# Optimization experiments

Hardware: AMD Instinct MI355X
Metric: run time of the kernel (lower is better)

Reference implementation:

```python
import jax, jax.numpy as jnp
import numpy as np

EMBED = 512
HEADS = 8
HEAD_DIM = EMBED // HEADS
N, T = 512, 64


def setup_inputs() -> dict:
    key = jax.random.key(0)
    ks = jax.random.split(key, 11)
    s = 1.0 / np.sqrt(EMBED)
    inp = {
        'values': jax.random.normal(ks[0], (N, T, EMBED), jnp.float32),
        'keys':   jax.random.normal(ks[1], (N, T, EMBED), jnp.float32),
        'query':  jax.random.normal(ks[2], (N, T, EMBED), jnp.float32),
        'Wv': jax.random.uniform(ks[3], (EMBED, EMBED), jnp.float32, -s, s),
        'bv': jax.random.uniform(ks[4], (EMBED,), jnp.float32, -s, s),
        'Wk': jax.random.uniform(ks[5], (EMBED, EMBED), jnp.float32, -s, s),
        'bk': jax.random.uniform(ks[6], (EMBED,), jnp.float32, -s, s),
        'Wq': jax.random.uniform(ks[7], (EMBED, EMBED), jnp.float32, -s, s),
        'bq': jax.random.uniform(ks[8], (EMBED,), jnp.float32, -s, s),
        'Wo': jax.random.uniform(ks[9], (EMBED, EMBED), jnp.float32, -s, s),
        'bo': jax.random.uniform(ks[10], (EMBED,), jnp.float32, -s, s),
    }
    return inp


def reference(values, keys, query, Wv, bv, Wk, bk, Wq, bq, Wo, bo):
    n, t, c = query.shape
    v = (values @ Wv.T + bv).reshape(n, t, HEADS, HEAD_DIM)
    k = (keys   @ Wk.T + bk).reshape(n, t, HEADS, HEAD_DIM)
    q = (query  @ Wq.T + bq).reshape(n, t, HEADS, HEAD_DIM)
    # attention over the batch axis: energy[q,k,t,h]
    energy = jnp.einsum('qthd,kthd->qkth', q, k)
    attn = jax.nn.softmax(energy / jnp.sqrt(jnp.float32(EMBED)), axis=1)
    out = jnp.einsum('qkth,kthd->qthd', attn, v).reshape(n, t, HEADS * HEAD_DIM)
    return out @ Wo.T + bo
```

## Files before the change

### kernel.cpp

```cpp
#include <hip/hip_runtime.h>
#include <hip/hip_bf16.h>
#include <math.h>

#define NBATCH 512
#define TT 64
#define EMB 512
#define NHEADS 8
#define HDIM 64
#define MROWS (NBATCH * TT)
#define ROWSTRIDE (TT * EMB)
#define WSEG 262144

static constexpr float QSCALE = 0.0637587140f;

typedef __attribute__((ext_vector_type(8))) short short8v;
typedef __attribute__((ext_vector_type(4))) float f32x4;

__device__ __forceinline__ unsigned short f2bf(float x) {
    union { float f; unsigned int u; } v; v.f = x;
    unsigned int r = v.u + 0x7fff + ((v.u >> 16) & 1);
    return (unsigned short)(r >> 16);
}

__device__ __forceinline__ unsigned int cvtpk(float lo, float hi) {
    unsigned int r;
    asm("v_cvt_pk_bf16_f32 %0, %1, %2" : "=v"(r) : "v"(lo), "v"(hi));
    return r;
}

__device__ __forceinline__ void gl16(const void* g, void* l) {
    __builtin_amdgcn_global_load_lds(
        (const __attribute__((address_space(1))) unsigned int*)g,
        (__attribute__((address_space(3))) unsigned int*)l, 16, 0, 0);
}

__global__ __launch_bounds__(256) void cvtw(
    const float* __restrict__ w0, const float* __restrict__ w1,
    const float* __restrict__ w2, const float* __restrict__ w3,
    unsigned short* __restrict__ dst)
{
    const int seg = blockIdx.y;
    const float* src = (seg == 0) ? w0 : (seg == 1) ? w1 : (seg == 2) ? w2 : w3;
    const float sc = (seg == 0) ? QSCALE : 1.0f;
    const size_t i = (size_t)blockIdx.x * 256 + threadIdx.x;
    float4 v = reinterpret_cast<const float4*>(src)[i];
    ushort4 r;
    r.x = f2bf(v.x * sc); r.y = f2bf(v.y * sc); r.z = f2bf(v.z * sc); r.w = f2bf(v.w * sc);
    reinterpret_cast<ushort4*>(dst + (size_t)seg * WSEG)[i] = r;
}

__global__ __launch_bounds__(512) void gemm_proj3(
    const float* __restrict__ A0, const float* __restrict__ A1,
    const float* __restrict__ A2, const unsigned short* __restrict__ Wb,
    const float* __restrict__ b0, const float* __restrict__ b1, const float* __restrict__ b2,
    unsigned short* __restrict__ o0, unsigned short* __restrict__ o1, unsigned short* __restrict__ o2)
{
    __shared__ __align__(16) float Asf[128 * 64];
    __shared__ __align__(16) unsigned short Bs[512 * 64];
    const int z = blockIdx.y;
    const float* A = (z == 0) ? A0 : (z == 1) ? A1 : A2;
    const unsigned short* W = Wb + (size_t)z * WSEG;
    const float* bias = (z == 0) ? b0 : (z == 1) ? b1 : b2;
    const float bsc = (z == 0) ? QSCALE : 1.0f;
    unsigned short* Cout = (z == 0) ? o0 : (z == 1) ? o1 : o2;

    const int tid = threadIdx.x;
    const int wave = tid >> 6, lane = tid & 63;
    const int lg = lane >> 4, li = lane & 15;
    const int m0 = blockIdx.x * 128;
    const int wm = (wave >> 2) * 64;
    const int wn = (wave & 3) * 128;

    f32x4 acc[4][8] = {};

    const int au = (tid & 15) ^ ((tid >> 4) & 15);
    const float* gaf = A + (size_t)(m0 + (tid >> 4)) * 512 + au * 4;
    float* lA = Asf + wave * 256;
    const unsigned short* gb = W + (size_t)(tid >> 3) * 512 + (tid & 7) * 8;
    unsigned short* lB = Bs + wave * 512;

    for (int k0 = 0; k0 < 512; k0 += 64) {
        __syncthreads();
#pragma unroll
        for (int i = 0; i < 4; i++)
            gl16(gaf + k0 + (size_t)i * 32 * 512, lA + i * 2048);
#pragma unroll
        for (int i = 0; i < 8; i++)
            gl16(gb + k0 + (size_t)i * 64 * 512, lB + i * 4096);
        __syncthreads();

#pragma unroll
        for (int kk = 0; kk < 2; kk++) {
            short8v af[4];
#pragma unroll
            for (int i = 0; i < 4; i++) {
                const int r = wm + i * 16 + li;
                const int lu0 = kk * 8 + lg * 2;
                const float4 fa = *reinterpret_cast<const float4*>(
                    &Asf[r * 64 + (lu0 ^ li) * 4]);
                const float4 fb = *reinterpret_cast<const float4*>(
                    &Asf[r * 64 + ((lu0 + 1) ^ li) * 4]);
                union { unsigned int u[4]; short8v v; } pk;
                pk.u[0] = cvtpk(fa.x, fa.y); pk.u[1] = cvtpk(fa.z, fa.w);
                pk.u[2] = cvtpk(fb.x, fb.y); pk.u[3] = cvtpk(fb.z, fb.w);
                af[i] = pk.v;
            }
#pragma unroll
            for (int j = 0; j < 8; j++) {
                const short8v bfr = *reinterpret_cast<const short8v*>(
                    &Bs[(wn + j * 16 + li) * 64 + kk * 32 + lg * 8]);
#pragma unroll
                for (int i = 0; i < 4; i++)
                    acc[i][j] = __builtin_amdgcn_mfma_f32_16x16x32_bf16(af[i], bfr, acc[i][j], 0, 0, 0);
            }
        }
    }

#pragma unroll
    for (int j = 0; j < 8; j++) {
        const int col = wn + j * 16 + li;
        const float bb = bias[col] * bsc;
#pragma unroll
        for (int i = 0; i < 4; i++) {
            const int row0 = m0 + wm + i * 16 + lg * 4;
#pragma unroll
            for (int r = 0; r < 4; r++)
                Cout[(size_t)(row0 + r) * 512 + col] = f2bf(acc[i][j][r] + bb);
        }
    }
}

__global__ __launch_bounds__(256) void gemm_out(
    const unsigned short* __restrict__ A, const unsigned short* __restrict__ W,
    const float* __restrict__ bias, float* __restrict__ Cout)
{
    __shared__ __align__(16) unsigned short As[128 * 32];
    __shared__ __align__(16) unsigned short Bs[128 * 32];
    const int tid = threadIdx.x;
    const int wave = tid >> 6, lane = tid & 63;
    const int lg = lane >> 4, li = lane & 15;
    const int m0 = blockIdx.x * 128;
    const int n0 = blockIdx.y * 128;
    const int wr = (wave >> 1) * 64;
    const int wc = (wave & 1) * 64;

    f32x4 acc[4][4] = {};

    const unsigned short* ga = A + (size_t)(m0 + (tid >> 2)) * 512 + (tid & 3) * 8;
    const unsigned short* gb = W + (size_t)(n0 + (tid >> 2)) * 512 + (tid & 3) * 8;
    unsigned short* lA = &As[wave * 512];
    unsigned short* lB = &Bs[wave * 512];

    for (int k0 = 0; k0 < 512; k0 += 32) {
        __syncthreads();
        gl16(ga + k0, lA);
        gl16(ga + k0 + 64 * 512, lA + 2048);
        gl16(gb + k0, lB);
        gl16(gb + k0 + 64 * 512, lB + 2048);
        __syncthreads();

        short8v af[4], bfr[4];
#pragma unroll
        for (int i = 0; i < 4; i++) {
            af[i]  = *reinterpret_cast<const short8v*>(&As[(wr + i * 16 + li) * 32 + lg * 8]);
            bfr[i] = *reinterpret_cast<const short8v*>(&Bs[(wc + i * 16 + li) * 32 + lg * 8]);
        }
#pragma unroll
        for (int i = 0; i < 4; i++)
#pragma unroll
            for (int j = 0; j < 4; j++)
                acc[i][j] = __builtin_amdgcn_mfma_f32_16x16x32_bf16(af[i], bfr[j], acc[i][j], 0, 0, 0);
    }

#pragma unroll
    for (int j = 0; j < 4; j++) {
        const int col = n0 + wc + j * 16 + li;
        const float bb = bias[col];
#pragma unroll
        for (int i = 0; i < 4; i++) {
            const int row0 = m0 + wr + i * 16 + lg * 4;
#pragma unroll
            for (int r = 0; r < 4; r++)
                Cout[(size_t)(row0 + r) * 512 + col] = acc[i][j][r] + bb;
        }
    }
}

__global__ __launch_bounds__(256) void attn_bf16(
    const unsigned short* __restrict__ qp, const unsigned short* __restrict__ kp,
    const unsigned short* __restrict__ vp, unsigned short* __restrict__ ao)
{
    __shared__ __align__(16) unsigned short Qs[128 * 64];
    __shared__ __align__(16) unsigned short Ks[64 * 64];
    __shared__ __align__(16) unsigned short Vt[64][68];
    __shared__ __align__(16) unsigned short Pl[4][32][72];

    const int tid = threadIdx.x;
    const int wave = tid >> 6, lane = tid & 63;
    const int lg = lane >> 4, li = lane & 15;
    const int n0 = blockIdx.x * 128;
    const int th = blockIdx.y;
    const size_t base = (size_t)(th >> 3) * EMB + (size_t)(th & 7) * HDIM;

    {
        const unsigned short* gq = qp + (size_t)(n0 + (tid >> 3)) * ROWSTRIDE + base + (tid & 7) * 8;
        unsigned short* lq = &Qs[wave * 512];
#pragma unroll
        for (int i = 0; i < 4; i++)
            gl16(gq + (size_t)i * 32 * ROWSTRIDE, lq + i * 2048);
    }
    __syncthreads();
    short8v qf[2][2];
#pragma unroll
    for (int mf = 0; mf < 2; mf++)
#pragma unroll
        for (int kf = 0; kf < 2; kf++)
            qf[mf][kf] = *reinterpret_cast<const short8v*>(
                &Qs[(wave * 32 + mf * 16 + li) * 64 + kf * 32 + lg * 8]);

    const int vd0 = (tid & 15) * 4;
    const int vk0 = (tid >> 4) * 4;
    const unsigned short* gv = vp + base + vd0;
    uint2 vl[4];
#pragma unroll
    for (int i = 0; i < 4; i++)
        vl[i] = *reinterpret_cast<const uint2*>(gv + (size_t)(vk0 + i) * ROWSTRIDE);

    const short8v ones = (short8v)(short)0x3F80;
    f32x4 acc[2][4] = {};
    f32x4 acc_l[2] = {};

    for (int kv = 0; kv < 8; kv++) {
        const int k0 = kv * 64;
        __syncthreads();

        {
            unsigned short* lk = &Ks[wave * 512];
#pragma unroll
            for (int i = 0; i < 2; i++) {
                const int r = (tid >> 3) + i * 32;
                const int srcofs = (((tid & 7) * 8) ^ ((r & 7) * 8));
                gl16(kp + (size_t)(k0 + r) * ROWSTRIDE + base + srcofs, lk + i * 2048);
            }
        }
#pragma unroll
        for (int dd = 0; dd < 4; dd++) {
            const unsigned int sel = (dd & 1) ? 0x07060302u : 0x05040100u;
            const unsigned int a = (dd < 2) ? vl[0].x : vl[0].y;
            const unsigned int b = (dd < 2) ? vl[1].x : vl[1].y;
            const unsigned int c = (dd < 2) ? vl[2].x : vl[2].y;
            const unsigned int d = (dd < 2) ? vl[3].x : vl[3].y;
            uint2 o;
            o.x = __builtin_amdgcn_perm(b, a, sel);
            o.y = __builtin_amdgcn_perm(d, c, sel);
            *reinterpret_cast<uint2*>(&Vt[vd0 + dd][vk0]) = o;
        }
        __syncthreads();

        if (kv < 7) {
#pragma unroll
            for (int i = 0; i < 4; i++)
                vl[i] = *reinterpret_cast<const uint2*>(
                    gv + (size_t)(k0 + 64 + vk0 + i) * ROWSTRIDE);
        }

        f32x4 s[2][4] = {};
#pragma unroll
        for (int nf = 0; nf < 4; nf++) {
            const int key = nf * 16 + li;
#pragma unroll
            for (int kf = 0; kf < 2; kf++) {
                const short8v kfrag = *reinterpret_cast<const short8v*>(
                    &Ks[key * 64 + ((kf * 32 + lg * 8) ^ ((key & 7) * 8))]);
#pragma unroll
                for (int mf = 0; mf < 2; mf++)
                    s[mf][nf] = __builtin_amdgcn_mfma_f32_16x16x32_bf16(kfrag, qf[mf][kf], s[mf][nf], 0, 0, 0);
            }
        }

#pragma unroll
        for (int mf = 0; mf < 2; mf++)
#pragma unroll
            for (int nf = 0; nf < 4; nf++) {
                const float p0 = exp2f(s[mf][nf][0]);
                const float p1 = exp2f(s[mf][nf][1]);
                const float p2 = exp2f(s[mf][nf][2]);
                const float p3 = exp2f(s[mf][nf][3]);
                union { unsigned int u[2]; uint2 v; } pk2;
                pk2.u[0] = cvtpk(p0, p1);
                pk2.u[1] = cvtpk(p2, p3);
                *reinterpret_cast<uint2*>(&Pl[wave][mf * 16 + li][nf * 16 + lg * 4]) = pk2.v;
            }

        short8v pf[2][2];
#pragma unroll
        for (int mf = 0; mf < 2; mf++)
#pragma unroll
            for (int kf = 0; kf < 2; kf++)
                pf[mf][kf] = *reinterpret_cast<const short8v*>(
                    &Pl[wave][mf * 16 + li][kf * 32 + lg * 8]);
#pragma unroll
        for (int mf = 0; mf < 2; mf++)
#pragma unroll
            for (int kf = 0; kf < 2; kf++)
                acc_l[mf] = __builtin_amdgcn_mfma_f32_16x16x32_bf16(pf[mf][kf], ones, acc_l[mf], 0, 0, 0);

#pragma unroll
        for (int df = 0; df < 4; df++)
#pragma unroll
            for (int kf = 0; kf < 2; kf++) {
                const short8v vfr = *reinterpret_cast<const short8v*>(
                    &Vt[df * 16 + li][kf * 32 + lg * 8]);
#pragma unroll
                for (int mf = 0; mf < 2; mf++)
                    acc[mf][df] = __builtin_amdgcn_mfma_f32_16x16x32_bf16(pf[mf][kf], vfr, acc[mf][df], 0, 0, 0);
            }
    }

#pragma unroll
    for (int mf = 0; mf < 2; mf++) {
#pragma unroll
        for (int r = 0; r < 4; r++) {
            const float linv = 1.0f / acc_l[mf][r];
            const int qrow = n0 + wave * 32 + mf * 16 + lg * 4 + r;
#pragma unroll
            for (int df = 0; df < 4; df++)
                ao[(size_t)qrow * ROWSTRIDE + base + df * 16 + li] = f2bf(acc[mf][df][r] * linv);
        }
    }
}

extern "C" void kernel_launch(void* const* d_in, const int* in_sizes, int n_in,
                              void* d_out, int out_size, void* d_ws, size_t ws_size,
                              hipStream_t stream) {
    const float* values = (const float*)d_in[0];
    const float* keys   = (const float*)d_in[1];
    const float* query  = (const float*)d_in[2];
    const float* Wv = (const float*)d_in[3];
    const float* bv = (const float*)d_in[4];
    const float* Wk = (const float*)d_in[5];
    const float* bk = (const float*)d_in[6];
    const float* Wq = (const float*)d_in[7];
    const float* bq = (const float*)d_in[8];
    const float* Wo = (const float*)d_in[9];
    const float* bo = (const float*)d_in[10];
    float* out = (float*)d_out;

    unsigned short* ws16 = (unsigned short*)d_ws;
    const size_t PLANE = (size_t)MROWS * EMB;
    unsigned short* qb = ws16;
    unsigned short* kb = ws16 + PLANE;
    unsigned short* vb = ws16 + 2 * PLANE;
    unsigned short* ab = ws16 + 3 * PLANE;
    unsigned short* wb = ws16 + 4 * PLANE;

    cvtw<<<dim3(WSEG / 4 / 256, 4), 256, 0, stream>>>(Wq, Wk, Wv, Wo, wb);

    gemm_proj3<<<dim3(MROWS / 128, 3), 512, 0, stream>>>(
        query, keys, values, wb, bq, bk, bv, qb, kb, vb);

    attn_bf16<<<dim3(4, TT * NHEADS), 256, 0, stream>>>(qb, kb, vb, ab);

    gemm_out<<<dim3(MROWS / 128, EMB / 128), 256, 0, stream>>>(
        ab, wb + 3 * WSEG, bo, out);
}
```

Before: 223.8 us.

## Double-buffer projection GEMM with register-prefetched bf16 A tiles

Restructures the fused QKV projection GEMM main loop to use K=32 double-buffered LDS tiles. The next W tile is prefetched asynchronously and the next A tile goes through registers while MFMAs run on the current buffer. A is now converted to bf16 once when stored to LDS rather than converted from fp32 on every fragment read, which halves A's LDS footprint. Each iteration now needs one barrier instead of two, so global loads overlap with compute, at the cost of more register pressure and more, smaller loop iterations.

Result: slower. 228.7 us (+2.2%).

```diff
diff --git a/kernel.cpp b/kernel.cpp
--- a/kernel.cpp
+++ b/kernel.cpp
@@ -55,8 +55,8 @@
     const float* __restrict__ b0, const float* __restrict__ b1, const float* __restrict__ b2,
     unsigned short* __restrict__ o0, unsigned short* __restrict__ o1, unsigned short* __restrict__ o2)
 {
-    __shared__ __align__(16) float Asf[128 * 64];
-    __shared__ __align__(16) unsigned short Bs[512 * 64];
+    __shared__ __align__(16) unsigned short Ws[2][512 * 32];
+    __shared__ __align__(16) unsigned short Ab[2][128 * 32];
     const int z = blockIdx.y;
     const float* A = (z == 0) ? A0 : (z == 1) ? A1 : A2;
     const unsigned short* W = Wb + (size_t)z * WSEG;
@@ -73,47 +73,63 @@
 
     f32x4 acc[4][8] = {};
 
-    const int au = (tid & 15) ^ ((tid >> 4) & 15);
-    const float* gaf = A + (size_t)(m0 + (tid >> 4)) * 512 + au * 4;
-    float* lA = Asf + wave * 256;
-    const unsigned short* gb = W + (size_t)(tid >> 3) * 512 + (tid & 7) * 8;
-    unsigned short* lB = Bs + wave * 512;
-
-    for (int k0 = 0; k0 < 512; k0 += 64) {
-        __syncthreads();
+    const unsigned short* gw = W + (size_t)(tid >> 2) * 512
+                             + (size_t)(((tid & 3) ^ ((tid >> 2) & 3))) * 8;
+    const float* ga = A + (size_t)(m0 + (tid >> 2)) * 512 + (tid & 3) * 8;
+    const int awr = tid >> 2;
+    const int awu = (tid & 3) ^ (awr & 3);
+
+    {
 #pragma unroll
         for (int i = 0; i < 4; i++)
-            gl16(gaf + k0 + (size_t)i * 32 * 512, lA + i * 2048);
-#pragma unroll
-        for (int i = 0; i < 8; i++)
-            gl16(gb + k0 + (size_t)i * 64 * 512, lB + i * 4096);
-        __syncthreads();
-
-#pragma unroll
-        for (int kk = 0; kk < 2; kk++) {
-            short8v af[4];
-#pragma unroll
-            for (int i = 0; i < 4; i++) {
-                const int r = wm + i * 16 + li;
-                const int lu0 = kk * 8 + lg * 2;
-                const float4 fa = *reinterpret_cast<const float4*>(
-                    &Asf[r * 64 + (lu0 ^ li) * 4]);
-                const float4 fb = *reinterpret_cast<const float4*>(
-                    &Asf[r * 64 + ((lu0 + 1) ^ li) * 4]);
-                union { unsigned int u[4]; short8v v; } pk;
-                pk.u[0] = cvtpk(fa.x, fa.y); pk.u[1] = cvtpk(fa.z, fa.w);
-                pk.u[2] = cvtpk(fb.x, fb.y); pk.u[3] = cvtpk(fb.z, fb.w);
-                af[i] = pk.v;
-            }
-#pragma unroll
-            for (int j = 0; j < 8; j++) {
-                const short8v bfr = *reinterpret_cast<const short8v*>(
-                    &Bs[(wn + j * 16 + li) * 64 + kk * 32 + lg * 8]);
-#pragma unroll
-                for (int i = 0; i < 4; i++)
-                    acc[i][j] = __builtin_amdgcn_mfma_f32_16x16x32_bf16(af[i], bfr, acc[i][j], 0, 0, 0);
-            }
-        }
+            gl16(gw + (size_t)i * 128 * 512, &Ws[0][wave * 512 + i * 4096]);
+        const float4 f0 = *reinterpret_cast<const float4*>(ga);
+        const float4 f1 = *reinterpret_cast<const float4*>(ga + 4);
+        union { unsigned int u[4]; short8v v; } pk;
+        pk.u[0] = cvtpk(f0.x, f0.y); pk.u[1] = cvtpk(f0.z, f0.w);
+        pk.u[2] = cvtpk(f1.x, f1.y); pk.u[3] = cvtpk(f1.z, f1.w);
+        *reinterpret_cast<short8v*>(&Ab[0][awr * 32 + awu * 8]) = pk.v;
+    }
+    __syncthreads();
+
+    int cur = 0;
+    for (int t = 0; t < 16; ++t) {
+        const int k0 = t * 32;
+        float4 fn0, fn1;
+        if (t < 15) {
+#pragma unroll
+            for (int i = 0; i < 4; i++)
+                gl16(gw + k0 + 32 + (size_t)i * 128 * 512,
+                     &Ws[cur ^ 1][wave * 512 + i * 4096]);
+            fn0 = *reinterpret_cast<const float4*>(ga + k0 + 32);
+            fn1 = *reinterpret_cast<const float4*>(ga + k0 + 36);
+        }
+
+        short8v af[4];
+#pragma unroll
+        for (int i = 0; i < 4; i++) {
+            const int r = wm + i * 16 + li;
+            af[i] = *reinterpret_cast<const short8v*>(
+                &Ab[cur][r * 32 + (lg ^ (r & 3)) * 8]);
+        }
+#pragma unroll
+        for (int j = 0; j < 8; j++) {
+            const int R = wn + j * 16 + li;
+            const short8v bfr = *reinterpret_cast<const short8v*>(
+                &Ws[cur][R * 32 + (lg ^ (R & 3)) * 8]);
+#pragma unroll
+            for (int i = 0; i < 4; i++)
+                acc[i][j] = __builtin_amdgcn_mfma_f32_16x16x32_bf16(af[i], bfr, acc[i][j], 0, 0, 0);
+        }
+
+        if (t < 15) {
+            union { unsigned int u[4]; short8v v; } pk;
+            pk.u[0] = cvtpk(fn0.x, fn0.y); pk.u[1] = cvtpk(fn0.z, fn0.w);
+            pk.u[2] = cvtpk(fn1.x, fn1.y); pk.u[3] = cvtpk(fn1.z, fn1.w);
+            *reinterpret_cast<short8v*>(&Ab[cur ^ 1][awr * 32 + awu * 8]) = pk.v;
+        }
+        __syncthreads();
+        cur ^= 1;
     }
 
 #pragma unroll
```

## Double query rows per attention block and load Q fragments directly from global

Applied to the files above, without the earlier changes.

Each attention block now handles 256 query rows instead of 128, with each wave owning 64 rows. That halves the number of blocks that reload the same K/V tiles for a (t,h) pair. Q fragments are loaded straight from global memory into registers, so the Q shared-memory staging buffer and its barrier are gone. The K and V fragments are hoisted and reused across the four row groups, and the P scratch buffer shrinks to one 16-row tile processed per group. In exchange the grid is half as large (1024 blocks) and register pressure per wave is much higher, which may reduce occupancy.

Result: no change. 222.7 us (-0.5%).

```diff
diff --git a/kernel.cpp b/kernel.cpp
--- a/kernel.cpp
+++ b/kernel.cpp
@@ -190,33 +190,25 @@
     const unsigned short* __restrict__ qp, const unsigned short* __restrict__ kp,
     const unsigned short* __restrict__ vp, unsigned short* __restrict__ ao)
 {
-    __shared__ __align__(16) unsigned short Qs[128 * 64];
     __shared__ __align__(16) unsigned short Ks[64 * 64];
     __shared__ __align__(16) unsigned short Vt[64][68];
-    __shared__ __align__(16) unsigned short Pl[4][32][72];
+    __shared__ __align__(16) unsigned short Pl[4][16][72];
 
     const int tid = threadIdx.x;
     const int wave = tid >> 6, lane = tid & 63;
     const int lg = lane >> 4, li = lane & 15;
-    const int n0 = blockIdx.x * 128;
+    const int n0 = blockIdx.x * 256;
     const int th = blockIdx.y;
     const size_t base = (size_t)(th >> 3) * EMB + (size_t)(th & 7) * HDIM;
 
-    {
-        const unsigned short* gq = qp + (size_t)(n0 + (tid >> 3)) * ROWSTRIDE + base + (tid & 7) * 8;
-        unsigned short* lq = &Qs[wave * 512];
-#pragma unroll
-        for (int i = 0; i < 4; i++)
-            gl16(gq + (size_t)i * 32 * ROWSTRIDE, lq + i * 2048);
-    }
-    __syncthreads();
-    short8v qf[2][2];
-#pragma unroll
-    for (int mf = 0; mf < 2; mf++)
+    short8v qf[4][2];
+#pragma unroll
+    for (int mf = 0; mf < 4; mf++)
 #pragma unroll
         for (int kf = 0; kf < 2; kf++)
             qf[mf][kf] = *reinterpret_cast<const short8v*>(
-                &Qs[(wave * 32 + mf * 16 + li) * 64 + kf * 32 + lg * 8]);
+                qp + (size_t)(n0 + wave * 64 + mf * 16 + li) * ROWSTRIDE
+                   + base + kf * 32 + lg * 8);
 
     const int vd0 = (tid & 15) * 4;
     const int vk0 = (tid >> 4) * 4;
@@ -227,8 +219,8 @@
         vl[i] = *reinterpret_cast<const uint2*>(gv + (size_t)(vk0 + i) * ROWSTRIDE);
 
     const short8v ones = (short8v)(short)0x3F80;
-    f32x4 acc[2][4] = {};
-    f32x4 acc_l[2] = {};
+    f32x4 acc[4][4] = {};
+    f32x4 acc_l[4] = {};
 
     for (int kv = 0; kv < 8; kv++) {
         const int k0 = kv * 64;
@@ -264,65 +256,65 @@
                     gv + (size_t)(k0 + 64 + vk0 + i) * ROWSTRIDE);
         }
 
-        f32x4 s[2][4] = {};
+        short8v kfr[4][2], vfr[4][2];
 #pragma unroll
         for (int nf = 0; nf < 4; nf++) {
             const int key = nf * 16 + li;
 #pragma unroll
-            for (int kf = 0; kf < 2; kf++) {
-                const short8v kfrag = *reinterpret_cast<const short8v*>(
+            for (int kf = 0; kf < 2; kf++)
+                kfr[nf][kf] = *reinterpret_cast<const short8v*>(
                     &Ks[key * 64 + ((kf * 32 + lg * 8) ^ ((key & 7) * 8))]);
-#pragma unroll
-                for (int mf = 0; mf < 2; mf++)
-                    s[mf][nf] = __builtin_amdgcn_mfma_f32_16x16x32_bf16(kfrag, qf[mf][kf], s[mf][nf], 0, 0, 0);
-            }
-        }
-
-#pragma unroll
-        for (int mf = 0; mf < 2; mf++)
+        }
+#pragma unroll
+        for (int df = 0; df < 4; df++)
+#pragma unroll
+            for (int kf = 0; kf < 2; kf++)
+                vfr[df][kf] = *reinterpret_cast<const short8v*>(
+                    &Vt[df * 16 + li][kf * 32 + lg * 8]);
+
+#pragma unroll
+        for (int mf = 0; mf < 4; mf++) {
+            f32x4 s[4] = {};
+#pragma unroll
+            for (int nf = 0; nf < 4; nf++)
+#pragma unroll
+                for (int kf = 0; kf < 2; kf++)
+                    s[nf] = __builtin_amdgcn_mfma_f32_16x16x32_bf16(kfr[nf][kf], qf[mf][kf], s[nf], 0, 0, 0);
+
 #pragma unroll
             for (int nf = 0; nf < 4; nf++) {
-                const float p0 = exp2f(s[mf][nf][0]);
-                const float p1 = exp2f(s[mf][nf][1]);
-                const float p2 = exp2f(s[mf][nf][2]);
-                const float p3 = exp2f(s[mf][nf][3]);
+                const float p0 = exp2f(s[nf][0]);
+                const float p1 = exp2f(s[nf][1]);
+                const float p2 = exp2f(s[nf][2]);
+                const float p3 = exp2f(s[nf][3]);
                 union { unsigned int u[2]; uint2 v; } pk2;
                 pk2.u[0] = cvtpk(p0, p1);
                 pk2.u[1] = cvtpk(p2, p3);
-                *reinterpret_cast<uint2*>(&Pl[wave][mf * 16 + li][nf * 16 + lg * 4]) = pk2.v;
+                *reinterpret_cast<uint2*>(&Pl[wave][li][nf * 16 + lg * 4]) = pk2.v;
             }
 
-        short8v pf[2][2];
-#pragma unroll
-        for (int mf = 0; mf < 2; mf++)
+            short8v pf[2];
 #pragma unroll
             for (int kf = 0; kf < 2; kf++)
-                pf[mf][kf] = *reinterpret_cast<const short8v*>(
-                    &Pl[wave][mf * 16 + li][kf * 32 + lg * 8]);
-#pragma unroll
-        for (int mf = 0; mf < 2; mf++)
+                pf[kf] = *reinterpret_cast<const short8v*>(
+                    &Pl[wave][li][kf * 32 + lg * 8]);
 #pragma unroll
             for (int kf = 0; kf < 2; kf++)
-                acc_l[mf] = __builtin_amdgcn_mfma_f32_16x16x32_bf16(pf[mf][kf], ones, acc_l[mf], 0, 0, 0);
-
-#pragma unroll
-        for (int df = 0; df < 4; df++)
-#pragma unroll
-            for (int kf = 0; kf < 2; kf++) {
-                const short8v vfr = *reinterpret_cast<const short8v*>(
-                    &Vt[df * 16 + li][kf * 32 + lg * 8]);
-#pragma unroll
-                for (int mf = 0; mf < 2; mf++)
-                    acc[mf][df] = __builtin_amdgcn_mfma_f32_16x16x32_bf16(pf[mf][kf], vfr, acc[mf][df], 0, 0, 0);
-            }
-    }
-
-#pragma unroll
-    for (int mf = 0; mf < 2; mf++) {
+                acc_l[mf] = __builtin_amdgcn_mfma_f32_16x16x32_bf16(pf[kf], ones, acc_l[mf], 0, 0, 0);
+#pragma unroll
+            for (int df = 0; df < 4; df++)
+#pragma unroll
+                for (int kf = 0; kf < 2; kf++)
+                    acc[mf][df] = __builtin_amdgcn_mfma_f32_16x16x32_bf16(pf[kf], vfr[df][kf], acc[mf][df], 0, 0, 0);
+        }
+    }
+
+#pragma unroll
+    for (int mf = 0; mf < 4; mf++) {
 #pragma unroll
         for (int r = 0; r < 4; r++) {
             const float linv = 1.0f / acc_l[mf][r];
-            const int qrow = n0 + wave * 32 + mf * 16 + lg * 4 + r;
+            const int qrow = n0 + wave * 64 + mf * 16 + lg * 4 + r;
 #pragma unroll
             for (int df = 0; df < 4; df++)
                 ao[(size_t)qrow * ROWSTRIDE + base + df * 16 + li] = f2bf(acc[mf][df][r] * linv);
@@ -359,7 +351,7 @@
     gemm_proj3<<<dim3(MROWS / 128, 3), 512, 0, stream>>>(
         query, keys, values, wb, bq, bk, bv, qb, kb, vb);
 
-    attn_bf16<<<dim3(4, TT * NHEADS), 256, 0, stream>>>(qb, kb, vb, ab);
+    attn_bf16<<<dim3(2, TT * NHEADS), 256, 0, stream>>>(qb, kb, vb, ab);
 
     gemm_out<<<dim3(MROWS / 128, EMB / 128), 256, 0, stream>>>(
         ab, wb + 3 * WSEG, bo, out);
```
